# Optimization experiments

Measured on AMD Instinct MI355X. Metric: run time of the kernel, lower is better.

The kernel has to match this reference:

```python
import jax, jax.numpy as jnp
import numpy as np

EPS = 1e-6
B, T, D, A = 16, 2048, 512, 128
SCALE = A ** (-0.5)


def _xavier(key, fan_in, fan_out):
    limit = np.sqrt(6.0 / (fan_in + fan_out)).astype(np.float32)
    return jax.random.uniform(key, (fan_in, fan_out), jnp.float32, -limit, limit)


def setup_inputs() -> dict:
    key = jax.random.key(0)
    kx, kq, kk, kv = jax.random.split(key, 4)
    x = jax.random.normal(kx, (B, T, D), jnp.float32)
    Wq = _xavier(kq, D, A)
    Wk = _xavier(kk, D, A)
    Wv = _xavier(kv, D, 1)
    bq = jnp.full((A,), 0.01, jnp.float32)
    bk = jnp.full((A,), 0.01, jnp.float32)
    bv = jnp.full((1,), 0.01, jnp.float32)
    return {"x": x, "Wq": Wq, "bq": bq, "Wk": Wk, "bk": bk, "Wv": Wv, "bv": bv}


def reference(x, Wq, bq, Wk, bk, Wv, bv):
    # mean-variance norm over features (torch.std default is unbiased -> ddof=1)
    mu = jnp.mean(x, axis=-1, keepdims=True)
    sd = jnp.std(x, axis=-1, keepdims=True, ddof=1)
    xn = (x - mu) / (sd + EPS)
    Q = xn @ Wq + bq            # [B, T, A]
    K = xn @ Wk + bk            # [B, T, A]
    V = xn @ Wv + bv            # [B, T, 1]
    scores = jnp.einsum("bta,bsa->bts", Q, K) * SCALE  # [B, T, T]
    w_att = jax.nn.softmax(scores, axis=-1)
    w = jnp.einsum("bts,bso->bto", w_att, V)           # [B, T, 1]
    return (w, w_att)
```

## Files before the change

kernel.cpp:

```cpp
#include <hip/hip_runtime.h>

#define NB 16
#define NT 2048
#define ND 512
#define NA 128
#define EPSV 1e-6f
#define SCALE 0.08838834764831845f
#define NCH 4
#define SCH 512

typedef __bf16 bf16;
typedef __bf16 bf16x4 __attribute__((ext_vector_type(4)));
typedef __bf16 bf16x8 __attribute__((ext_vector_type(8)));
typedef float f32x4 __attribute__((ext_vector_type(4)));

__global__ void prep_wt(const float* __restrict__ Wq, const float* __restrict__ Wk,
                        bf16* __restrict__ WT) {
    int n = blockIdx.x;
    const float* W = (n < NA) ? Wq : Wk;
    int col = n & (NA - 1);
    for (int k = threadIdx.x; k < ND; k += blockDim.x)
        WT[(size_t)n * ND + k] = (bf16)W[(size_t)k * NA + col];
}

__launch_bounds__(256)
__global__ void norm_proj(const float* __restrict__ x, const float* __restrict__ Wv,
                          const float* __restrict__ bvp, const bf16* __restrict__ WT,
                          const float* __restrict__ bq, const float* __restrict__ bk,
                          bf16* __restrict__ QK, float* __restrict__ Vout) {
    __shared__ bf16 xn[16 * ND];
    const int tid = threadIdx.x;
    const int lane = tid & 63, wv = tid >> 6;
    const int row0 = blockIdx.x * 16;

    float wvv[8];
    float sumw = 0.f;
#pragma unroll
    for (int i = 0; i < 4; ++i) { wvv[i]     = Wv[lane * 4 + i];       sumw += wvv[i]; }
#pragma unroll
    for (int i = 0; i < 4; ++i) { wvv[4 + i] = Wv[256 + lane * 4 + i]; sumw += wvv[4 + i]; }
#pragma unroll
    for (int m = 1; m < 64; m <<= 1) sumw += __shfl_xor(sumw, m);
    const float bvs = bvp[0];

#pragma unroll
    for (int r = 0; r < 4; ++r) {
        const int lrow = wv * 4 + r;
        const int grow = row0 + lrow;
        const float* xr = x + (size_t)grow * ND;
        f32x4 a = *(const f32x4*)(xr + lane * 4);
        f32x4 b = *(const f32x4*)(xr + 256 + lane * 4);
        float s = 0.f, sq = 0.f, dw = 0.f;
#pragma unroll
        for (int i = 0; i < 4; ++i) { s += a[i]; sq += a[i] * a[i]; dw += a[i] * wvv[i]; }
#pragma unroll
        for (int i = 0; i < 4; ++i) { s += b[i]; sq += b[i] * b[i]; dw += b[i] * wvv[4 + i]; }
#pragma unroll
        for (int m = 1; m < 64; m <<= 1) {
            s  += __shfl_xor(s, m);
            sq += __shfl_xor(sq, m);
            dw += __shfl_xor(dw, m);
        }
        const float mu  = s * (1.f / 512.f);
        float var = (sq - 512.f * mu * mu) * (1.f / 511.f);
        var = fmaxf(var, 0.f);
        const float inv = 1.f / (sqrtf(var) + EPSV);
        if (lane == 0) Vout[grow] = (dw - mu * sumw) * inv + bvs;

        const int sw = (lrow & 7) << 4;
        bf16x4 v0, v1;
#pragma unroll
        for (int i = 0; i < 4; ++i) v0[i] = (bf16)((a[i] - mu) * inv);
#pragma unroll
        for (int i = 0; i < 4; ++i) v1[i] = (bf16)((b[i] - mu) * inv);
        *(bf16x4*)((char*)xn + lrow * 1024 + ((lane * 8) ^ sw))       = v0;
        *(bf16x4*)((char*)xn + lrow * 1024 + ((512 + lane * 8) ^ sw)) = v1;
    }
    __syncthreads();

    const int c = lane & 15, g = lane >> 4;
    const int asw = (c & 7) << 4;
    f32x4 acc[4];
#pragma unroll
    for (int i = 0; i < 4; ++i) acc[i] = f32x4{0.f, 0.f, 0.f, 0.f};

    for (int ks = 0; ks < 16; ++ks) {
        const bf16x8 af = *(const bf16x8*)((const char*)xn + c * 1024 +
                                           ((ks * 64 + g * 16) ^ asw));
#pragma unroll
        for (int i = 0; i < 4; ++i) {
            const int n = wv * 64 + i * 16 + c;
            const bf16x8 bfr = *(const bf16x8*)(WT + (size_t)n * ND + ks * 32 + g * 8);
            acc[i] = __builtin_amdgcn_mfma_f32_16x16x32_bf16(af, bfr, acc[i], 0, 0, 0);
        }
    }
#pragma unroll
    for (int i = 0; i < 4; ++i) {
        const int n = wv * 64 + i * 16 + c;
        const float bias = (n < NA) ? bq[n] : bk[n - NA];
#pragma unroll
        for (int j = 0; j < 4; ++j)
            QK[(size_t)(row0 + g * 4 + j) * 256 + n] = (bf16)(acc[i][j] + bias);
    }
}

__launch_bounds__(256)
__global__ void attn_pass1(const bf16* __restrict__ QK, const float* __restrict__ Vg,
                           float* __restrict__ pl, float* __restrict__ pw) {
    __shared__ bf16 Kt[64 * NA];
    const int tid = threadIdx.x;
    const int lane = tid & 63, wv = tid >> 6;
    const int b = blockIdx.z, t0 = blockIdx.x * 64, sc = blockIdx.y;
    const int c = lane & 15, g = lane >> 4;
    const int trow = t0 + wv * 16 + c;

    bf16x8 qf[4];
    const bf16* qrow = QK + (size_t)(b * NT + trow) * 256;
#pragma unroll
    for (int ks = 0; ks < 4; ++ks) qf[ks] = *(const bf16x8*)(qrow + ks * 32 + g * 8);

    const int srow = tid >> 4, scc = tid & 15;
    const bf16* kbase = QK + (size_t)(b * NT + sc * SCH + srow) * 256 + NA + scc * 8;
    bf16* kdst = (bf16*)((char*)Kt + srow * 256 + ((scc * 16) ^ ((srow & 7) << 4)));
    bf16x8 sreg[4];

#pragma unroll
    for (int i = 0; i < 4; ++i)
        sreg[i] = *(const bf16x8*)(kbase + (size_t)(i * 16) * 256);

    const float* vbase = Vg + b * NT + sc * SCH;
    float l_loc = 0.f, w_loc = 0.f;

    for (int tt = 0; tt < SCH / 64; ++tt) {
        __syncthreads();
#pragma unroll
        for (int i = 0; i < 4; ++i)
            *(bf16x8*)((char*)kdst + i * 16 * 256) = sreg[i];
        if (tt + 1 < SCH / 64) {
            const bf16* nb = kbase + (size_t)(tt + 1) * 64 * 256;
#pragma unroll
            for (int i = 0; i < 4; ++i)
                sreg[i] = *(const bf16x8*)(nb + (size_t)(i * 16) * 256);
        }
        __syncthreads();

#pragma unroll
        for (int ns = 0; ns < 4; ++ns) {
            f32x4 acc = f32x4{0.f, 0.f, 0.f, 0.f};
            const int rr = ns * 16 + c;
            const int rsw = (rr & 7) << 4;
#pragma unroll
            for (int ks = 0; ks < 4; ++ks) {
                const bf16x8 afr = *(const bf16x8*)((const char*)Kt + rr * 256 +
                                                    ((ks * 64 + g * 16) ^ rsw));
                acc = __builtin_amdgcn_mfma_f32_16x16x32_bf16(afr, qf[ks], acc, 0, 0, 0);
            }
            const f32x4 vv = *(const f32x4*)(vbase + tt * 64 + ns * 16 + g * 4);
#pragma unroll
            for (int jj = 0; jj < 4; ++jj) {
                const float p = __expf(acc[jj] * SCALE);
                l_loc += p;
                w_loc += p * vv[jj];
            }
        }
    }

#pragma unroll
    for (int mask = 16; mask <= 32; mask <<= 1) {
        l_loc += __shfl_xor(l_loc, mask);
        w_loc += __shfl_xor(w_loc, mask);
    }
    if (g == 0) {
        const int idx = sc * (NB * NT) + b * NT + trow;
        pl[idx] = l_loc;
        pw[idx] = w_loc;
    }
}

__global__ void attn_reduce(const float* __restrict__ pl, const float* __restrict__ pw,
                            float* __restrict__ linv, float* __restrict__ out_w) {
    const int r = blockIdx.x * 256 + threadIdx.x;
    float L = 0.f, W = 0.f;
#pragma unroll
    for (int ch = 0; ch < NCH; ++ch) {
        L += pl[ch * (NB * NT) + r];
        W += pw[ch * (NB * NT) + r];
    }
    linv[r] = 1.f / L;
    out_w[r] = W / L;
}

__launch_bounds__(256)
__global__ void attn_pass2(const bf16* __restrict__ QK, const float* __restrict__ linv,
                           float* __restrict__ out_att) {
    __shared__ bf16 Kt[64 * NA];
    const int tid = threadIdx.x;
    const int lane = tid & 63, wv = tid >> 6;
    const int b = blockIdx.z, t0 = blockIdx.x * 64, sc = blockIdx.y;
    const int c = lane & 15, g = lane >> 4;
    const int trow = t0 + wv * 16 + c;

    bf16x8 qf[4];
    const bf16* qrow = QK + (size_t)(b * NT + trow) * 256;
#pragma unroll
    for (int ks = 0; ks < 4; ++ks) qf[ks] = *(const bf16x8*)(qrow + ks * 32 + g * 8);

    const int srow = tid >> 4, scc = tid & 15;
    const bf16* kbase = QK + (size_t)(b * NT + sc * SCH + srow) * 256 + NA + scc * 8;
    bf16* kdst = (bf16*)((char*)Kt + srow * 256 + ((scc * 16) ^ ((srow & 7) << 4)));
    bf16x8 sreg[4];

#pragma unroll
    for (int i = 0; i < 4; ++i)
        sreg[i] = *(const bf16x8*)(kbase + (size_t)(i * 16) * 256);

    const float lrow = linv[b * NT + trow];
    float* orow = out_att + (size_t)(b * NT + trow) * NT;

    for (int tt = 0; tt < SCH / 64; ++tt) {
        __syncthreads();
#pragma unroll
        for (int i = 0; i < 4; ++i)
            *(bf16x8*)((char*)kdst + i * 16 * 256) = sreg[i];
        if (tt + 1 < SCH / 64) {
            const bf16* nb = kbase + (size_t)(tt + 1) * 64 * 256;
#pragma unroll
            for (int i = 0; i < 4; ++i)
                sreg[i] = *(const bf16x8*)(nb + (size_t)(i * 16) * 256);
        }
        __syncthreads();

        const int s0 = sc * SCH + tt * 64;
#pragma unroll
        for (int ns = 0; ns < 4; ++ns) {
            f32x4 acc = f32x4{0.f, 0.f, 0.f, 0.f};
            const int rr = ns * 16 + c;
            const int rsw = (rr & 7) << 4;
#pragma unroll
            for (int ks = 0; ks < 4; ++ks) {
                const bf16x8 afr = *(const bf16x8*)((const char*)Kt + rr * 256 +
                                                    ((ks * 64 + g * 16) ^ rsw));
                acc = __builtin_amdgcn_mfma_f32_16x16x32_bf16(afr, qf[ks], acc, 0, 0, 0);
            }
            f32x4 w;
#pragma unroll
            for (int jj = 0; jj < 4; ++jj)
                w[jj] = __expf(acc[jj] * SCALE) * lrow;
            *(f32x4*)(orow + s0 + ns * 16 + g * 4) = w;
        }
    }
}

extern "C" void kernel_launch(void* const* d_in, const int* in_sizes, int n_in,
                              void* d_out, int out_size, void* d_ws, size_t ws_size,
                              hipStream_t stream) {
    const float* x  = (const float*)d_in[0];
    const float* Wq = (const float*)d_in[1];
    const float* bq = (const float*)d_in[2];
    const float* Wk = (const float*)d_in[3];
    const float* bk = (const float*)d_in[4];
    const float* Wv = (const float*)d_in[5];
    const float* bv = (const float*)d_in[6];

    float* out_w   = (float*)d_out;
    float* out_att = (float*)d_out + NB * NT;

    char* ws = (char*)d_ws;
    bf16*  WT   = (bf16*)ws;
    float* V    = (float*)(ws + 262144);
    bf16*  QK   = (bf16*)(ws + 393216);
    float* pl   = (float*)(ws + 17170432);
    float* pw   = (float*)(ws + 17694720);
    float* linv = (float*)(ws + 18219008);

    prep_wt<<<dim3(256), dim3(256), 0, stream>>>(Wq, Wk, WT);
    norm_proj<<<dim3((NB * NT) / 16), dim3(256), 0, stream>>>(x, Wv, bv, WT, bq, bk, QK, V);
    attn_pass1<<<dim3(NT / 64, NCH, NB), dim3(256), 0, stream>>>(QK, V, pl, pw);
    attn_reduce<<<dim3((NB * NT) / 256), dim3(256), 0, stream>>>(pl, pw, linv, out_w);
    attn_pass2<<<dim3(NT / 64, NCH, NB), dim3(256), 0, stream>>>(QK, linv, out_att);
}
```

Before: 175.8 us.

## Keep K fragments in registers per wave, drop LDS staging and barriers

Both attention passes stop staging K tiles through shared memory with two barriers per iteration. Instead, each wave loads its own 16 K rows straight into registers (with a prefetch of the next tile) and computes against all 64 query rows held in registers. Pass1 adds a small shared-memory cross-wave reduction to combine per-wave partial sums. This removes LDS traffic and synchronisation but raises register pressure (launch bounds set to 3 blocks per SIMD), and pass2 now writes 16-column strips per wave, which changes the store pattern.

```diff
diff --git a/kernel.cpp b/kernel.cpp
--- a/kernel.cpp
+++ b/kernel.cpp
@@ -104,76 +104,84 @@
     }
 }
 
-__launch_bounds__(256)
+__launch_bounds__(256, 3)
 __global__ void attn_pass1(const bf16* __restrict__ QK, const float* __restrict__ Vg,
                            float* __restrict__ pl, float* __restrict__ pw) {
-    __shared__ bf16 Kt[64 * NA];
+    __shared__ float redl[4][64], redw[4][64];
     const int tid = threadIdx.x;
-    const int lane = tid & 63, wv = tid >> 6;
+    const int lane = tid & 63, w = tid >> 6;
     const int b = blockIdx.z, t0 = blockIdx.x * 64, sc = blockIdx.y;
     const int c = lane & 15, g = lane >> 4;
-    const int trow = t0 + wv * 16 + c;
-
-    bf16x8 qf[4];
-    const bf16* qrow = QK + (size_t)(b * NT + trow) * 256;
-#pragma unroll
-    for (int ks = 0; ks < 4; ++ks) qf[ks] = *(const bf16x8*)(qrow + ks * 32 + g * 8);
-
-    const int srow = tid >> 4, scc = tid & 15;
-    const bf16* kbase = QK + (size_t)(b * NT + sc * SCH + srow) * 256 + NA + scc * 8;
-    bf16* kdst = (bf16*)((char*)Kt + srow * 256 + ((scc * 16) ^ ((srow & 7) << 4)));
-    bf16x8 sreg[4];
-
-#pragma unroll
-    for (int i = 0; i < 4; ++i)
-        sreg[i] = *(const bf16x8*)(kbase + (size_t)(i * 16) * 256);
-
-    const float* vbase = Vg + b * NT + sc * SCH;
-    float l_loc = 0.f, w_loc = 0.f;
+
+    bf16x8 qf[4][4];
+#pragma unroll
+    for (int tb = 0; tb < 4; ++tb) {
+        const bf16* qrow = QK + (size_t)(b * NT + t0 + tb * 16 + c) * 256;
+#pragma unroll
+        for (int ks = 0; ks < 4; ++ks)
+            qf[tb][ks] = *(const bf16x8*)(qrow + ks * 32 + g * 8);
+    }
+
+    const bf16* kp = QK + (size_t)(b * NT + sc * SCH + w * 16 + c) * 256 + NA + g * 8;
+    const float* vp = Vg + b * NT + sc * SCH + w * 16 + g * 4;
+
+    bf16x8 kf[4], kfn[4];
+#pragma unroll
+    for (int ks = 0; ks < 4; ++ks) kf[ks] = *(const bf16x8*)(kp + ks * 32);
+
+    float l_loc[4] = {0.f, 0.f, 0.f, 0.f}, w_loc[4] = {0.f, 0.f, 0.f, 0.f};
 
     for (int tt = 0; tt < SCH / 64; ++tt) {
-        __syncthreads();
-#pragma unroll
-        for (int i = 0; i < 4; ++i)
-            *(bf16x8*)((char*)kdst + i * 16 * 256) = sreg[i];
         if (tt + 1 < SCH / 64) {
-            const bf16* nb = kbase + (size_t)(tt + 1) * 64 * 256;
-#pragma unroll
-            for (int i = 0; i < 4; ++i)
-                sreg[i] = *(const bf16x8*)(nb + (size_t)(i * 16) * 256);
-        }
-        __syncthreads();
-
-#pragma unroll
-        for (int ns = 0; ns < 4; ++ns) {
-            f32x4 acc = f32x4{0.f, 0.f, 0.f, 0.f};
-            const int rr = ns * 16 + c;
-            const int rsw = (rr & 7) << 4;
-#pragma unroll
-            for (int ks = 0; ks < 4; ++ks) {
-                const bf16x8 afr = *(const bf16x8*)((const char*)Kt + rr * 256 +
-                                                    ((ks * 64 + g * 16) ^ rsw));
-                acc = __builtin_amdgcn_mfma_f32_16x16x32_bf16(afr, qf[ks], acc, 0, 0, 0);
+#pragma unroll
+            for (int ks = 0; ks < 4; ++ks)
+                kfn[ks] = *(const bf16x8*)(kp + (size_t)(tt + 1) * 64 * 256 + ks * 32);
+        }
+        const f32x4 vv = *(const f32x4*)(vp + tt * 64);
+        f32x4 acc[4];
+#pragma unroll
+        for (int tb = 0; tb < 4; ++tb) acc[tb] = f32x4{0.f, 0.f, 0.f, 0.f};
+#pragma unroll
+        for (int tb = 0; tb < 4; ++tb)
+#pragma unroll
+            for (int ks = 0; ks < 4; ++ks)
+                acc[tb] = __builtin_amdgcn_mfma_f32_16x16x32_bf16(kf[ks], qf[tb][ks],
+                                                                  acc[tb], 0, 0, 0);
+#pragma unroll
+        for (int tb = 0; tb < 4; ++tb)
+#pragma unroll
+            for (int jj = 0; jj < 4; ++jj) {
+                const float p = __expf(acc[tb][jj] * SCALE);
+                l_loc[tb] += p;
+                w_loc[tb] += p * vv[jj];
             }
-            const f32x4 vv = *(const f32x4*)(vbase + tt * 64 + ns * 16 + g * 4);
-#pragma unroll
-            for (int jj = 0; jj < 4; ++jj) {
-                const float p = __expf(acc[jj] * SCALE);
-                l_loc += p;
-                w_loc += p * vv[jj];
-            }
-        }
-    }
-
-#pragma unroll
-    for (int mask = 16; mask <= 32; mask <<= 1) {
-        l_loc += __shfl_xor(l_loc, mask);
-        w_loc += __shfl_xor(w_loc, mask);
+#pragma unroll
+        for (int ks = 0; ks < 4; ++ks) kf[ks] = kfn[ks];
+    }
+
+#pragma unroll
+    for (int tb = 0; tb < 4; ++tb) {
+#pragma unroll
+        for (int mask = 16; mask <= 32; mask <<= 1) {
+            l_loc[tb] += __shfl_xor(l_loc[tb], mask);
+            w_loc[tb] += __shfl_xor(w_loc[tb], mask);
+        }
     }
     if (g == 0) {
-        const int idx = sc * (NB * NT) + b * NT + trow;
-        pl[idx] = l_loc;
-        pw[idx] = w_loc;
+#pragma unroll
+        for (int tb = 0; tb < 4; ++tb) {
+            redl[w][tb * 16 + c] = l_loc[tb];
+            redw[w][tb * 16 + c] = w_loc[tb];
+        }
+    }
+    __syncthreads();
+    if (tid < 64) {
+        float L = 0.f, W = 0.f;
+#pragma unroll
+        for (int ww = 0; ww < 4; ++ww) { L += redl[ww][tid]; W += redw[ww][tid]; }
+        const int idx = sc * (NB * NT) + b * NT + t0 + tid;
+        pl[idx] = L;
+        pw[idx] = W;
     }
 }
 
@@ -190,64 +198,58 @@
     out_w[r] = W / L;
 }
 
-__launch_bounds__(256)
+__launch_bounds__(256, 3)
 __global__ void attn_pass2(const bf16* __restrict__ QK, const float* __restrict__ linv,
                            float* __restrict__ out_att) {
-    __shared__ bf16 Kt[64 * NA];
     const int tid = threadIdx.x;
-    const int lane = tid & 63, wv = tid >> 6;
+    const int lane = tid & 63, w = tid >> 6;
     const int b = blockIdx.z, t0 = blockIdx.x * 64, sc = blockIdx.y;
     const int c = lane & 15, g = lane >> 4;
-    const int trow = t0 + wv * 16 + c;
-
-    bf16x8 qf[4];
-    const bf16* qrow = QK + (size_t)(b * NT + trow) * 256;
-#pragma unroll
-    for (int ks = 0; ks < 4; ++ks) qf[ks] = *(const bf16x8*)(qrow + ks * 32 + g * 8);
-
-    const int srow = tid >> 4, scc = tid & 15;
-    const bf16* kbase = QK + (size_t)(b * NT + sc * SCH + srow) * 256 + NA + scc * 8;
-    bf16* kdst = (bf16*)((char*)Kt + srow * 256 + ((scc * 16) ^ ((srow & 7) << 4)));
-    bf16x8 sreg[4];
-
-#pragma unroll
-    for (int i = 0; i < 4; ++i)
-        sreg[i] = *(const bf16x8*)(kbase + (size_t)(i * 16) * 256);
-
-    const float lrow = linv[b * NT + trow];
-    float* orow = out_att + (size_t)(b * NT + trow) * NT;
+
+    bf16x8 qf[4][4];
+    float li[4];
+#pragma unroll
+    for (int tb = 0; tb < 4; ++tb) {
+        const bf16* qrow = QK + (size_t)(b * NT + t0 + tb * 16 + c) * 256;
+#pragma unroll
+        for (int ks = 0; ks < 4; ++ks)
+            qf[tb][ks] = *(const bf16x8*)(qrow + ks * 32 + g * 8);
+        li[tb] = linv[b * NT + t0 + tb * 16 + c];
+    }
+
+    const bf16* kp = QK + (size_t)(b * NT + sc * SCH + w * 16 + c) * 256 + NA + g * 8;
+
+    bf16x8 kf[4], kfn[4];
+#pragma unroll
+    for (int ks = 0; ks < 4; ++ks) kf[ks] = *(const bf16x8*)(kp + ks * 32);
+
+    float* obase = out_att + (size_t)(b * NT) * NT + sc * SCH + w * 16 + g * 4;
 
     for (int tt = 0; tt < SCH / 64; ++tt) {
-        __syncthreads();
-#pragma unroll
-        for (int i = 0; i < 4; ++i)
-            *(bf16x8*)((char*)kdst + i * 16 * 256) = sreg[i];
         if (tt + 1 < SCH / 64) {
-            const bf16* nb = kbase + (size_t)(tt + 1) * 64 * 256;
-#pragma unroll
-            for (int i = 0; i < 4; ++i)
-                sreg[i] = *(const bf16x8*)(nb + (size_t)(i * 16) * 256);
-        }
-        __syncthreads();
-
-        const int s0 = sc * SCH + tt * 64;
-#pragma unroll
-        for (int ns = 0; ns < 4; ++ns) {
-            f32x4 acc = f32x4{0.f, 0.f, 0.f, 0.f};
-            const int rr = ns * 16 + c;
-            const int rsw = (rr & 7) << 4;
-#pragma unroll
-            for (int ks = 0; ks < 4; ++ks) {
-                const bf16x8 afr = *(const bf16x8*)((const char*)Kt + rr * 256 +
-                                                    ((ks * 64 + g * 16) ^ rsw));
-                acc = __builtin_amdgcn_mfma_f32_16x16x32_bf16(afr, qf[ks], acc, 0, 0, 0);
-            }
-            f32x4 w;
+#pragma unroll
+            for (int ks = 0; ks < 4; ++ks)
+                kfn[ks] = *(const bf16x8*)(kp + (size_t)(tt + 1) * 64 * 256 + ks * 32);
+        }
+        f32x4 acc[4];
+#pragma unroll
+        for (int tb = 0; tb < 4; ++tb) acc[tb] = f32x4{0.f, 0.f, 0.f, 0.f};
+#pragma unroll
+        for (int tb = 0; tb < 4; ++tb)
+#pragma unroll
+            for (int ks = 0; ks < 4; ++ks)
+                acc[tb] = __builtin_amdgcn_mfma_f32_16x16x32_bf16(kf[ks], qf[tb][ks],
+                                                                  acc[tb], 0, 0, 0);
+#pragma unroll
+        for (int tb = 0; tb < 4; ++tb) {
+            f32x4 wv4;
 #pragma unroll
             for (int jj = 0; jj < 4; ++jj)
-                w[jj] = __expf(acc[jj] * SCALE) * lrow;
-            *(f32x4*)(orow + s0 + ns * 16 + g * 4) = w;
-        }
+                wv4[jj] = __expf(acc[tb][jj] * SCALE) * li[tb];
+            *(f32x4*)(obase + (size_t)(t0 + tb * 16 + c) * NT + tt * 64) = wv4;
+        }
+#pragma unroll
+        for (int ks = 0; ks < 4; ++ks) kf[ks] = kfn[ks];
     }
 }
 
```

Measured after the change: 207.8 us. 18.2% more time.

## Fuse softmax denominator reduction into pass2 and reorder attention grid

Applied to the files above, without the earlier changes.

Removes the separate attn_reduce kernel: each pass2 thread now sums the per-chunk partial denominators and weighted sums itself, and chunk 0 writes out_w. Pass1 splits the key range into 8 chunks of 256 instead of 4 of 512, which doubles the block count for better occupancy. Both attention grids now put the key-chunk index in blockIdx.x, so blocks sharing the same query rows run next to each other for cache locality. The cost is redundant partial-sum reads in every pass2 block and a larger partials buffer.

```diff
diff --git a/kernel.cpp b/kernel.cpp
--- a/kernel.cpp
+++ b/kernel.cpp
@@ -6,8 +6,10 @@
 #define NA 128
 #define EPSV 1e-6f
 #define SCALE 0.08838834764831845f
-#define NCH 4
-#define SCH 512
+#define NCH1 8
+#define SCH1 256
+#define NCH2 4
+#define SCH2 512
 
 typedef __bf16 bf16;
 typedef __bf16 bf16x4 __attribute__((ext_vector_type(4)));
@@ -110,7 +112,7 @@
     __shared__ bf16 Kt[64 * NA];
     const int tid = threadIdx.x;
     const int lane = tid & 63, wv = tid >> 6;
-    const int b = blockIdx.z, t0 = blockIdx.x * 64, sc = blockIdx.y;
+    const int sc = blockIdx.x, b = blockIdx.y, t0 = blockIdx.z * 64;
     const int c = lane & 15, g = lane >> 4;
     const int trow = t0 + wv * 16 + c;
 
@@ -120,7 +122,7 @@
     for (int ks = 0; ks < 4; ++ks) qf[ks] = *(const bf16x8*)(qrow + ks * 32 + g * 8);
 
     const int srow = tid >> 4, scc = tid & 15;
-    const bf16* kbase = QK + (size_t)(b * NT + sc * SCH + srow) * 256 + NA + scc * 8;
+    const bf16* kbase = QK + (size_t)(b * NT + sc * SCH1 + srow) * 256 + NA + scc * 8;
     bf16* kdst = (bf16*)((char*)Kt + srow * 256 + ((scc * 16) ^ ((srow & 7) << 4)));
     bf16x8 sreg[4];
 
@@ -128,19 +130,18 @@
     for (int i = 0; i < 4; ++i)
         sreg[i] = *(const bf16x8*)(kbase + (size_t)(i * 16) * 256);
 
-    const float* vbase = Vg + b * NT + sc * SCH;
+    const float* vbase = Vg + b * NT + sc * SCH1;
     float l_loc = 0.f, w_loc = 0.f;
 
-    for (int tt = 0; tt < SCH / 64; ++tt) {
+    for (int tt = 0; tt < SCH1 / 64; ++tt) {
         __syncthreads();
 #pragma unroll
         for (int i = 0; i < 4; ++i)
             *(bf16x8*)((char*)kdst + i * 16 * 256) = sreg[i];
-        if (tt + 1 < SCH / 64) {
-            const bf16* nb = kbase + (size_t)(tt + 1) * 64 * 256;
+        if (tt + 1 < SCH1 / 64) {
 #pragma unroll
             for (int i = 0; i < 4; ++i)
-                sreg[i] = *(const bf16x8*)(nb + (size_t)(i * 16) * 256);
+                sreg[i] = *(const bf16x8*)(kbase + (size_t)((tt + 1) * 64 + i * 16) * 256);
         }
         __syncthreads();
 
@@ -177,26 +178,14 @@
     }
 }
 
-__global__ void attn_reduce(const float* __restrict__ pl, const float* __restrict__ pw,
-                            float* __restrict__ linv, float* __restrict__ out_w) {
-    const int r = blockIdx.x * 256 + threadIdx.x;
-    float L = 0.f, W = 0.f;
-#pragma unroll
-    for (int ch = 0; ch < NCH; ++ch) {
-        L += pl[ch * (NB * NT) + r];
-        W += pw[ch * (NB * NT) + r];
-    }
-    linv[r] = 1.f / L;
-    out_w[r] = W / L;
-}
-
 __launch_bounds__(256)
-__global__ void attn_pass2(const bf16* __restrict__ QK, const float* __restrict__ linv,
+__global__ void attn_pass2(const bf16* __restrict__ QK, const float* __restrict__ pl,
+                           const float* __restrict__ pw, float* __restrict__ out_w,
                            float* __restrict__ out_att) {
     __shared__ bf16 Kt[64 * NA];
     const int tid = threadIdx.x;
     const int lane = tid & 63, wv = tid >> 6;
-    const int b = blockIdx.z, t0 = blockIdx.x * 64, sc = blockIdx.y;
+    const int sc = blockIdx.x, b = blockIdx.y, t0 = blockIdx.z * 64;
     const int c = lane & 15, g = lane >> 4;
     const int trow = t0 + wv * 16 + c;
 
@@ -205,8 +194,17 @@
 #pragma unroll
     for (int ks = 0; ks < 4; ++ks) qf[ks] = *(const bf16x8*)(qrow + ks * 32 + g * 8);
 
+    float L = 0.f, W = 0.f;
+#pragma unroll
+    for (int ch = 0; ch < NCH1; ++ch) {
+        L += pl[ch * (NB * NT) + b * NT + trow];
+        W += pw[ch * (NB * NT) + b * NT + trow];
+    }
+    const float lrow = 1.f / L;
+    if (sc == 0 && g == 0) out_w[b * NT + trow] = W * lrow;
+
     const int srow = tid >> 4, scc = tid & 15;
-    const bf16* kbase = QK + (size_t)(b * NT + sc * SCH + srow) * 256 + NA + scc * 8;
+    const bf16* kbase = QK + (size_t)(b * NT + sc * SCH2 + srow) * 256 + NA + scc * 8;
     bf16* kdst = (bf16*)((char*)Kt + srow * 256 + ((scc * 16) ^ ((srow & 7) << 4)));
     bf16x8 sreg[4];
 
@@ -214,23 +212,21 @@
     for (int i = 0; i < 4; ++i)
         sreg[i] = *(const bf16x8*)(kbase + (size_t)(i * 16) * 256);
 
-    const float lrow = linv[b * NT + trow];
     float* orow = out_att + (size_t)(b * NT + trow) * NT;
 
-    for (int tt = 0; tt < SCH / 64; ++tt) {
+    for (int tt = 0; tt < SCH2 / 64; ++tt) {
         __syncthreads();
 #pragma unroll
         for (int i = 0; i < 4; ++i)
             *(bf16x8*)((char*)kdst + i * 16 * 256) = sreg[i];
-        if (tt + 1 < SCH / 64) {
-            const bf16* nb = kbase + (size_t)(tt + 1) * 64 * 256;
+        if (tt + 1 < SCH2 / 64) {
 #pragma unroll
             for (int i = 0; i < 4; ++i)
-                sreg[i] = *(const bf16x8*)(nb + (size_t)(i * 16) * 256);
-        }
-        __syncthreads();
-
-        const int s0 = sc * SCH + tt * 64;
+                sreg[i] = *(const bf16x8*)(kbase + (size_t)((tt + 1) * 64 + i * 16) * 256);
+        }
+        __syncthreads();
+
+        const int s0 = sc * SCH2 + tt * 64;
 #pragma unroll
         for (int ns = 0; ns < 4; ++ns) {
             f32x4 acc = f32x4{0.f, 0.f, 0.f, 0.f};
@@ -266,16 +262,14 @@
     float* out_att = (float*)d_out + NB * NT;
 
     char* ws = (char*)d_ws;
-    bf16*  WT   = (bf16*)ws;
-    float* V    = (float*)(ws + 262144);
-    bf16*  QK   = (bf16*)(ws + 393216);
-    float* pl   = (float*)(ws + 17170432);
-    float* pw   = (float*)(ws + 17694720);
-    float* linv = (float*)(ws + 18219008);
+    bf16*  WT = (bf16*)ws;
+    float* V  = (float*)(ws + 262144);
+    bf16*  QK = (bf16*)(ws + 393216);
+    float* pl = (float*)(ws + 17170432);
+    float* pw = (float*)(ws + 18219008);
 
     prep_wt<<<dim3(256), dim3(256), 0, stream>>>(Wq, Wk, WT);
     norm_proj<<<dim3((NB * NT) / 16), dim3(256), 0, stream>>>(x, Wv, bv, WT, bq, bk, QK, V);
-    attn_pass1<<<dim3(NT / 64, NCH, NB), dim3(256), 0, stream>>>(QK, V, pl, pw);
-    attn_reduce<<<dim3((NB * NT) / 256), dim3(256), 0, stream>>>(pl, pw, linv, out_w);
-    attn_pass2<<<dim3(NT / 64, NCH, NB), dim3(256), 0, stream>>>(QK, linv, out_att);
-}
+    attn_pass1<<<dim3(NCH1, NB, NT / 64), dim3(256), 0, stream>>>(QK, V, pl, pw);
+    attn_pass2<<<dim3(NCH2, NB, NT / 64), dim3(256), 0, stream>>>(QK, pl, pw, out_w, out_att);
+}
```

After: 186.4 us. +6.0%, slower.

## Stash bf16 exp scores in output upper half, normalize instead of recomputing

Applied to the files above, without the earlier changes.

The first attention pass now also writes unnormalized exp scores as bf16 into the second half of each output row. The old second pass, which recomputed QK^T and exp, is replaced by a streaming kernel that reads those bf16 values, scales them by 1/L, and writes fp32 in place. This removes the duplicate matmul and exp work but adds an extra write and read of about 128MB, and rounding the scores to bf16 lowers output precision. The in-place write relies on each row being read fully into registers before it is overwritten, and the __syncthreads inside the row loop is there to order that.

```diff
diff --git a/kernel.cpp b/kernel.cpp
--- a/kernel.cpp
+++ b/kernel.cpp
@@ -105,8 +105,9 @@
 }
 
 __launch_bounds__(256)
-__global__ void attn_pass1(const bf16* __restrict__ QK, const float* __restrict__ Vg,
-                           float* __restrict__ pl, float* __restrict__ pw) {
+__global__ void scoreE(const bf16* __restrict__ QK, const float* __restrict__ Vg,
+                       float* __restrict__ pl, float* __restrict__ pw,
+                       float* __restrict__ out_att) {
     __shared__ bf16 Kt[64 * NA];
     const int tid = threadIdx.x;
     const int lane = tid & 63, wv = tid >> 6;
@@ -129,6 +130,7 @@
         sreg[i] = *(const bf16x8*)(kbase + (size_t)(i * 16) * 256);
 
     const float* vbase = Vg + b * NT + sc * SCH;
+    bf16* erow = (bf16*)(out_att + (size_t)(b * NT + trow) * NT) + NT + sc * SCH;
     float l_loc = 0.f, w_loc = 0.f;
 
     for (int tt = 0; tt < SCH / 64; ++tt) {
@@ -137,10 +139,9 @@
         for (int i = 0; i < 4; ++i)
             *(bf16x8*)((char*)kdst + i * 16 * 256) = sreg[i];
         if (tt + 1 < SCH / 64) {
-            const bf16* nb = kbase + (size_t)(tt + 1) * 64 * 256;
 #pragma unroll
             for (int i = 0; i < 4; ++i)
-                sreg[i] = *(const bf16x8*)(nb + (size_t)(i * 16) * 256);
+                sreg[i] = *(const bf16x8*)(kbase + (size_t)((tt + 1) * 64 + i * 16) * 256);
         }
         __syncthreads();
 
@@ -156,12 +157,15 @@
                 acc = __builtin_amdgcn_mfma_f32_16x16x32_bf16(afr, qf[ks], acc, 0, 0, 0);
             }
             const f32x4 vv = *(const f32x4*)(vbase + tt * 64 + ns * 16 + g * 4);
+            bf16x4 ev;
 #pragma unroll
             for (int jj = 0; jj < 4; ++jj) {
                 const float p = __expf(acc[jj] * SCALE);
                 l_loc += p;
                 w_loc += p * vv[jj];
+                ev[jj] = (bf16)p;
             }
+            *(bf16x4*)(erow + tt * 64 + ns * 16 + g * 4) = ev;
         }
     }
 
@@ -191,63 +195,22 @@
 }
 
 __launch_bounds__(256)
-__global__ void attn_pass2(const bf16* __restrict__ QK, const float* __restrict__ linv,
-                           float* __restrict__ out_att) {
-    __shared__ bf16 Kt[64 * NA];
+__global__ void normalizeE(const float* __restrict__ linv, float* __restrict__ out_att) {
     const int tid = threadIdx.x;
-    const int lane = tid & 63, wv = tid >> 6;
-    const int b = blockIdx.z, t0 = blockIdx.x * 64, sc = blockIdx.y;
-    const int c = lane & 15, g = lane >> 4;
-    const int trow = t0 + wv * 16 + c;
-
-    bf16x8 qf[4];
-    const bf16* qrow = QK + (size_t)(b * NT + trow) * 256;
-#pragma unroll
-    for (int ks = 0; ks < 4; ++ks) qf[ks] = *(const bf16x8*)(qrow + ks * 32 + g * 8);
-
-    const int srow = tid >> 4, scc = tid & 15;
-    const bf16* kbase = QK + (size_t)(b * NT + sc * SCH + srow) * 256 + NA + scc * 8;
-    bf16* kdst = (bf16*)((char*)Kt + srow * 256 + ((scc * 16) ^ ((srow & 7) << 4)));
-    bf16x8 sreg[4];
-
-#pragma unroll
-    for (int i = 0; i < 4; ++i)
-        sreg[i] = *(const bf16x8*)(kbase + (size_t)(i * 16) * 256);
-
-    const float lrow = linv[b * NT + trow];
-    float* orow = out_att + (size_t)(b * NT + trow) * NT;
-
-    for (int tt = 0; tt < SCH / 64; ++tt) {
+    for (int row = blockIdx.x; row < NB * NT; row += gridDim.x) {
+        float* orow = out_att + (size_t)row * NT;
+        const float li = linv[row];
+        const bf16* erow = (const bf16*)orow + NT;
+        const bf16x8 e = *(const bf16x8*)(erow + tid * 8);
         __syncthreads();
-#pragma unroll
-        for (int i = 0; i < 4; ++i)
-            *(bf16x8*)((char*)kdst + i * 16 * 256) = sreg[i];
-        if (tt + 1 < SCH / 64) {
-            const bf16* nb = kbase + (size_t)(tt + 1) * 64 * 256;
-#pragma unroll
-            for (int i = 0; i < 4; ++i)
-                sreg[i] = *(const bf16x8*)(nb + (size_t)(i * 16) * 256);
-        }
-        __syncthreads();
-
-        const int s0 = sc * SCH + tt * 64;
-#pragma unroll
-        for (int ns = 0; ns < 4; ++ns) {
-            f32x4 acc = f32x4{0.f, 0.f, 0.f, 0.f};
-            const int rr = ns * 16 + c;
-            const int rsw = (rr & 7) << 4;
-#pragma unroll
-            for (int ks = 0; ks < 4; ++ks) {
-                const bf16x8 afr = *(const bf16x8*)((const char*)Kt + rr * 256 +
-                                                    ((ks * 64 + g * 16) ^ rsw));
-                acc = __builtin_amdgcn_mfma_f32_16x16x32_bf16(afr, qf[ks], acc, 0, 0, 0);
-            }
-            f32x4 w;
-#pragma unroll
-            for (int jj = 0; jj < 4; ++jj)
-                w[jj] = __expf(acc[jj] * SCALE) * lrow;
-            *(f32x4*)(orow + s0 + ns * 16 + g * 4) = w;
-        }
+        f32x4 o0, o1;
+#pragma unroll
+        for (int i = 0; i < 4; ++i) {
+            o0[i] = (float)e[i] * li;
+            o1[i] = (float)e[4 + i] * li;
+        }
+        *(f32x4*)(orow + tid * 8)     = o0;
+        *(f32x4*)(orow + tid * 8 + 4) = o1;
     }
 }
 
@@ -275,7 +238,7 @@
 
     prep_wt<<<dim3(256), dim3(256), 0, stream>>>(Wq, Wk, WT);
     norm_proj<<<dim3((NB * NT) / 16), dim3(256), 0, stream>>>(x, Wv, bv, WT, bq, bk, QK, V);
-    attn_pass1<<<dim3(NT / 64, NCH, NB), dim3(256), 0, stream>>>(QK, V, pl, pw);
+    scoreE<<<dim3(NT / 64, NCH, NB), dim3(256), 0, stream>>>(QK, V, pl, pw, out_att);
     attn_reduce<<<dim3((NB * NT) / 256), dim3(256), 0, stream>>>(pl, pw, linv, out_w);
-    attn_pass2<<<dim3(NT / 64, NCH, NB), dim3(256), 0, stream>>>(QK, linv, out_att);
-}
+    normalizeE<<<dim3(2048), dim3(256), 0, stream>>>(linv, out_att);
+}
```

Measured after the change: 210.5 us. 19.8% more time.
